# Kernel tuning notes

Hardware: AMD Instinct MI355X
Metric: run time of the kernel (lower is better)

## Reference

```python
import jax, jax.numpy as jnp
import numpy as np

B, H, W, C = 16, 64, 64, 256
C8 = C // 8

def setup_inputs() -> dict:
    key = jax.random.key(0)
    ks = jax.random.split(key, 8)
    return {
        "x": jax.random.normal(ks[0], (B, H, W, C), dtype=jnp.float32),
        "Wf": jax.random.normal(ks[1], (C, C8), dtype=jnp.float32) * 0.05,
        "Wg": jax.random.normal(ks[2], (C, C8), dtype=jnp.float32) * 0.05,
        "Wh": jax.random.normal(ks[3], (C, C), dtype=jnp.float32) * 0.05,
        "bf": jax.random.normal(ks[4], (C8,), dtype=jnp.float32) * 0.05,
        "bg": jax.random.normal(ks[5], (C8,), dtype=jnp.float32) * 0.05,
        "bh": jax.random.normal(ks[6], (C,), dtype=jnp.float32) * 0.05,
        "gamma": jax.random.normal(ks[7], (1,), dtype=jnp.float32) * 0.05,
    }

def reference(x, Wf, Wg, Wh, bf, bg, bh, gamma):
    # 1x1 convs == per-pixel channel matmuls (NHWC)
    f = jnp.einsum('bhwc,cd->bhwd', x, Wf) + bf  # [B,H,W,C/8]
    g = jnp.einsum('bhwc,cd->bhwd', x, Wg) + bg  # [B,H,W,C/8]
    h = jnp.einsum('bhwc,cd->bhwd', x, Wh) + bh  # [B,H,W,C]
    b = x.shape[0]
    # K.batch_flatten flattens all non-batch dims -> attention over BATCH dim
    gf = g.reshape(b, -1)                      # [B, HWC/8]
    ff = f.reshape(b, -1)                      # [B, HWC/8]
    hf = h.reshape(b, -1)                      # [B, HWC]
    s = gf @ ff.T                              # [B, B]
    beta = jax.nn.softmax(s, axis=-1)          # softmax over batch axis
    o = (beta @ hf).reshape(x.shape)           # [B,H,W,C]
    # activation=None -> linear; gamma-scaled residual
    return gamma * o + x
```

## Files before the change

kernel.cpp:

```cpp
#include <hip/hip_runtime.h>

typedef __attribute__((ext_vector_type(4))) float  f4;
typedef __attribute__((ext_vector_type(8))) short  short8;
typedef __attribute__((ext_vector_type(4))) float  f32x4;
typedef __attribute__((ext_vector_type(2))) unsigned int u32x2;

static __device__ __forceinline__ unsigned short f2bf(float f) {
    unsigned u = __builtin_bit_cast(unsigned, f);
    unsigned r = (u + 0x7FFFu + ((u >> 16) & 1u)) >> 16;
    return (unsigned short)r;
}
static __device__ __forceinline__ float bf2f(unsigned short h) {
    return __builtin_bit_cast(float, ((unsigned)h) << 16);
}

__global__ __launch_bounds__(256) void k_setup(const float* __restrict__ Wh,
                                               const float* __restrict__ bh,
                                               const float* __restrict__ Wf,
                                               const float* __restrict__ Wg,
                                               const float* __restrict__ gamma,
                                               unsigned short* __restrict__ WhT,
                                               float* __restrict__ gb,
                                               unsigned short* __restrict__ Wfg_hi,
                                               unsigned short* __restrict__ Wfg_lo) {
    __shared__ float T[8 * 260];
    const int t = threadIdx.x, b = blockIdx.x;
    const float g = gamma[0];
    if (b < 32) {
        const int c0 = b * 8;
        const int cr = t >> 5, q = t & 31;
        f4 v0 = *(const f4*)(Wh + (c0 + cr) * 256 + q * 8);
        f4 v1 = *(const f4*)(Wh + (c0 + cr) * 256 + q * 8 + 4);
        *(f4*)(T + cr * 260 + q * 8)     = v0;
        *(f4*)(T + cr * 260 + q * 8 + 4) = v1;
        __syncthreads();
        short8 o;
        #pragma unroll
        for (int j = 0; j < 8; ++j) o[j] = (short)f2bf(g * T[j * 260 + t]);
        *(short8*)(WhT + t * 256 + c0) = o;
    } else {
        gb[t] = g * bh[t];
        const int n = t >> 2, cq = t & 3;
        const float* Wsrc = (n < 32) ? Wf : Wg;
        const int nn = n & 31;
        #pragma unroll
        for (int c8 = 0; c8 < 8; ++c8) {
            short8 h8, l8;
            #pragma unroll
            for (int k = 0; k < 8; ++k) {
                const int c = cq * 64 + c8 * 8 + k;
                const float v = Wsrc[c * 32 + nn];
                const unsigned short h = f2bf(v);
                h8[k] = (short)h;
                l8[k] = (short)f2bf(v - bf2f(h));
            }
            *(short8*)(Wfg_hi + n * 256 + cq * 64 + c8 * 8) = h8;
            *(short8*)(Wfg_lo + n * 256 + cq * 64 + c8 * 8) = l8;
        }
    }
}

__global__ __launch_bounds__(256, 2) void ka(const float* __restrict__ x,
                                             const unsigned short* __restrict__ Wfg_hi,
                                             const unsigned short* __restrict__ Wfg_lo,
                                             const float* __restrict__ bfv,
                                             const float* __restrict__ bgv,
                                             float* __restrict__ s_part) {
    __shared__ __align__(16) unsigned char smem[65536];

    const int t = threadIdx.x, w = t >> 6, l = t & 63;
    const int p = blockIdx.x * 4 + w;

    f4 xr[16];
    #pragma unroll
    for (int j = 0; j < 16; ++j)
        xr[j] = *(const f4*)(x + (((j << 12) + p) << 8) + l * 4);
    #pragma unroll
    for (int j = 0; j < 16; ++j) {
        const int r = j * 4 + w;
        int bo = r * 512 + l * 8;
        bo ^= (r & 7) << 4;
        const unsigned short h0 = f2bf(xr[j][0]), h1 = f2bf(xr[j][1]);
        const unsigned short h2 = f2bf(xr[j][2]), h3 = f2bf(xr[j][3]);
        u32x2 ph, pl;
        ph[0] = ((unsigned)h1 << 16) | h0;
        ph[1] = ((unsigned)h3 << 16) | h2;
        const unsigned short e0 = f2bf(xr[j][0] - bf2f(h0));
        const unsigned short e1 = f2bf(xr[j][1] - bf2f(h1));
        const unsigned short e2 = f2bf(xr[j][2] - bf2f(h2));
        const unsigned short e3 = f2bf(xr[j][3] - bf2f(h3));
        pl[0] = ((unsigned)e1 << 16) | e0;
        pl[1] = ((unsigned)e3 << 16) | e2;
        *(u32x2*)(smem + bo)         = ph;
        *(u32x2*)(smem + 32768 + bo) = pl;
    }
    __syncthreads();

    const int lrow = l & 15;
    const int kfe  = (l >> 4) * 8;
    const int ncol = w * 16 + lrow;
    f32x4 acc[4];
    #pragma unroll
    for (int mt = 0; mt < 4; ++mt) acc[mt] = (f32x4){0.f, 0.f, 0.f, 0.f};

    #pragma unroll
    for (int k0 = 0; k0 < 256; k0 += 32) {
        const short8 bh_ = *(const short8*)(Wfg_hi + ncol * 256 + k0 + kfe);
        const short8 bl_ = *(const short8*)(Wfg_lo + ncol * 256 + k0 + kfe);
        short8 ah[4], al[4];
        #pragma unroll
        for (int mt = 0; mt < 4; ++mt) {
            const int row = mt * 16 + lrow;
            int bo = row * 512 + (k0 + kfe) * 2;
            bo ^= (row & 7) << 4;
            ah[mt] = *(const short8*)(smem + bo);
            al[mt] = *(const short8*)(smem + 32768 + bo);
        }
        #pragma unroll
        for (int mt = 0; mt < 4; ++mt) {
            acc[mt] = __builtin_amdgcn_mfma_f32_16x16x32_bf16(ah[mt], bh_, acc[mt], 0, 0, 0);
            acc[mt] = __builtin_amdgcn_mfma_f32_16x16x32_bf16(al[mt], bh_, acc[mt], 0, 0, 0);
            acc[mt] = __builtin_amdgcn_mfma_f32_16x16x32_bf16(ah[mt], bl_, acc[mt], 0, 0, 0);
        }
    }
    __syncthreads();

    float* FG = (float*)smem;
    const float bias = (ncol < 32) ? bfv[ncol] : bgv[ncol - 32];
    #pragma unroll
    for (int mt = 0; mt < 4; ++mt)
        #pragma unroll
        for (int jj = 0; jj < 4; ++jj) {
            const int row = mt * 16 + (l >> 4) * 4 + jj;
            FG[row * 68 + ncol] = acc[mt][jj] + bias;
        }
    __syncthreads();

    const int si = t >> 4, sj = t & 15;
    float sacc = 0.f;
    #pragma unroll
    for (int q = 0; q < 4; ++q) {
        const float* Gp = FG + (si * 4 + q) * 68 + 32;
        const float* Fp = FG + (sj * 4 + q) * 68;
        #pragma unroll
        for (int d4 = 0; d4 < 8; ++d4) {
            f4 gv = *(const f4*)(Gp + d4 * 4);
            f4 fv = *(const f4*)(Fp + d4 * 4);
            sacc += gv[0] * fv[0] + gv[1] * fv[1] + gv[2] * fv[2] + gv[3] * fv[3];
        }
    }
    s_part[blockIdx.x * 256 + si * 16 + sj] = sacc;
}

__global__ __launch_bounds__(256) void kb1(const float* __restrict__ s_part,
                                           float* __restrict__ s_red) {
    const int t = threadIdx.x, b = blockIdx.x;
    float a = 0.f;
    #pragma unroll
    for (int k = 0; k < 16; ++k) a += s_part[(b * 16 + k) * 256 + t];
    s_red[b * 256 + t] = a;
}

__global__ __launch_bounds__(1024) void kb2(const float* __restrict__ s_red,
                                            float* __restrict__ beta) {
    __shared__ float red[4 * 256];
    __shared__ float srow[256];
    __shared__ float erow[256];
    const int t = threadIdx.x;
    const int pair = t & 255;
    const int qr = t >> 8;
    float a = 0.f;
    #pragma unroll
    for (int b = qr * 16; b < qr * 16 + 16; ++b) a += s_red[b * 256 + pair];
    red[qr * 256 + pair] = a;
    __syncthreads();
    float s = 0.f, e = 0.f;
    if (t < 256) {
        s = red[pair] + red[256 + pair] + red[512 + pair] + red[768 + pair];
        srow[pair] = s;
    }
    __syncthreads();
    if (t < 256) {
        const int i = pair >> 4;
        float m = srow[i * 16];
        #pragma unroll
        for (int j = 1; j < 16; ++j) m = fmaxf(m, srow[i * 16 + j]);
        e = expf(s - m);
        erow[pair] = e;
    }
    __syncthreads();
    if (t < 256) {
        const int i = pair >> 4;
        float sum = 0.f;
        #pragma unroll
        for (int j = 0; j < 16; ++j) sum += erow[i * 16 + j];
        beta[pair] = e / sum;
    }
}

__global__ __launch_bounds__(256, 2) void kc(const float* __restrict__ x,
                                             const unsigned short* __restrict__ WhT,
                                             const float* __restrict__ gb,
                                             const float* __restrict__ beta,
                                             float* __restrict__ out) {
    __shared__ __align__(16) unsigned char smem[33024];

    const int t = threadIdx.x;
    const int w = t >> 6;
    const int l = t & 63;
    const int p0 = blockIdx.x * 4;
    const int p  = p0 + w;
    const int cbase = l * 4;

    f4 xr[16];
    #pragma unroll
    for (int j = 0; j < 16; ++j)
        xr[j] = *(const f4*)(x + (((j << 12) + p) << 8) + cbase);
    #pragma unroll
    for (int i = 0; i < 16; ++i) {
        f4 a = {0.f, 0.f, 0.f, 0.f};
        #pragma unroll
        for (int j = 0; j < 16; ++j) {
            const float bij = beta[i * 16 + j];
            a += xr[j] * bij;
        }
        const int r = i * 4 + w;
        int bo = r * 512 + l * 8;
        bo ^= (r & 7) << 4;
        u32x2 packed;
        packed[0] = ((unsigned)f2bf(a[1]) << 16) | f2bf(a[0]);
        packed[1] = ((unsigned)f2bf(a[3]) << 16) | f2bf(a[2]);
        *(u32x2*)(smem + bo) = packed;
    }
    __syncthreads();

    f32x4 acc[4][4];
    #pragma unroll
    for (int mt = 0; mt < 4; ++mt)
        #pragma unroll
        for (int nt = 0; nt < 4; ++nt) acc[mt][nt] = (f32x4){0.f, 0.f, 0.f, 0.f};

    const int n0 = w * 64;
    const int lrow = l & 15;
    const int hi = l >> 4;
    const int kf = hi * 8;
    #pragma unroll
    for (int k0 = 0; k0 < 256; k0 += 32) {
        short8 af[4], bfr[4];
        #pragma unroll
        for (int mt = 0; mt < 4; ++mt) {
            const int row = mt * 16 + lrow;
            int bo = row * 512 + (k0 + kf) * 2;
            bo ^= (row & 7) << 4;
            af[mt] = *(const short8*)(smem + bo);
        }
        #pragma unroll
        for (int nt = 0; nt < 4; ++nt) {
            const int d = n0 + nt * 16 + lrow;
            bfr[nt] = *(const short8*)(WhT + d * 256 + k0 + kf);
        }
        #pragma unroll
        for (int mt = 0; mt < 4; ++mt)
            #pragma unroll
            for (int nt = 0; nt < 4; ++nt)
                acc[mt][nt] = __builtin_amdgcn_mfma_f32_16x16x32_bf16(
                    af[mt], bfr[nt], acc[mt][nt], 0, 0, 0);
    }

    float* cst = (float*)smem;
    const f4 gb4 = *(const f4*)(gb + cbase);
    #pragma unroll
    for (int h = 0; h < 2; ++h) {
        __syncthreads();
        #pragma unroll
        for (int mt2 = 0; mt2 < 2; ++mt2) {
            const int mt = h * 2 + mt2;
            #pragma unroll
            for (int nt = 0; nt < 4; ++nt)
                #pragma unroll
                for (int j = 0; j < 4; ++j) {
                    const int rl = mt2 * 16 + hi * 4 + j;
                    cst[rl * 258 + n0 + nt * 16 + lrow] = acc[mt][nt][j];
                }
        }
        __syncthreads();
        #pragma unroll
        for (int rr = 0; rr < 8; ++rr) {
            const int rl = rr * 4 + w;
            const int i  = h * 8 + rr;
            f4 o = *(const f4*)(cst + rl * 258 + cbase);
            o += gb4 + xr[i];
            *(f4*)(out + (((i << 12) + p) << 8) + cbase) = o;
        }
    }
}

extern "C" void kernel_launch(void* const* d_in, const int* in_sizes, int n_in,
                              void* d_out, int out_size, void* d_ws, size_t ws_size,
                              hipStream_t stream) {
    const float* x     = (const float*)d_in[0];
    const float* Wf    = (const float*)d_in[1];
    const float* Wg    = (const float*)d_in[2];
    const float* Wh    = (const float*)d_in[3];
    const float* bfv   = (const float*)d_in[4];
    const float* bgv   = (const float*)d_in[5];
    const float* bhv   = (const float*)d_in[6];
    const float* gamma = (const float*)d_in[7];
    float* out = (float*)d_out;

    char* ws = (char*)d_ws;
    unsigned short* WhT = (unsigned short*)ws;
    float* gb     = (float*)(ws + 131072);
    float* beta   = (float*)(ws + 132096);
    float* s_part = (float*)(ws + 133120);
    unsigned short* Wfg_hi = (unsigned short*)(ws + 1181696);
    unsigned short* Wfg_lo = (unsigned short*)(ws + 1214464);
    float* s_red  = (float*)(ws + 1181696);

    k_setup<<<dim3(33), dim3(256), 0, stream>>>(Wh, bhv, Wf, Wg, gamma, WhT, gb, Wfg_hi, Wfg_lo);
    ka<<<dim3(1024), dim3(256), 0, stream>>>(x, Wfg_hi, Wfg_lo, bfv, bgv, s_part);
    kb1<<<dim3(64), dim3(256), 0, stream>>>(s_part, s_red);
    kb2<<<dim3(1), dim3(1024), 0, stream>>>(s_red, beta);
    kc<<<dim3(1024), dim3(256), 0, stream>>>(x, WhT, gb, beta, out);
}
```

Baseline: 86.61 us.

## Halve kc tile to two pixels per block to raise occupancy

The final kernel now processes 2 pixels per block instead of 4, doubling the grid, halving shared memory, and raising launch bounds to 5 blocks per SM. x is no longer held in registers across the GEMM; the residual is re-read from global memory in the epilogue, and output uses nontemporal stores. This trades a second read of x and twice the WhT fetches per pixel for lower register and LDS pressure and more waves in flight.

```diff
diff --git a/kernel.cpp b/kernel.cpp
--- a/kernel.cpp
+++ b/kernel.cpp
@@ -1,6 +1,7 @@
 #include <hip/hip_runtime.h>
 
 typedef __attribute__((ext_vector_type(4))) float  f4;
+typedef __attribute__((ext_vector_type(2))) float  f2;
 typedef __attribute__((ext_vector_type(8))) short  short8;
 typedef __attribute__((ext_vector_type(4))) float  f32x4;
 typedef __attribute__((ext_vector_type(2))) unsigned int u32x2;
@@ -198,57 +199,57 @@
     }
 }
 
-__global__ __launch_bounds__(256, 2) void kc(const float* __restrict__ x,
+__global__ __launch_bounds__(256, 5) void kc(const float* __restrict__ x,
                                              const unsigned short* __restrict__ WhT,
                                              const float* __restrict__ gb,
                                              const float* __restrict__ beta,
                                              float* __restrict__ out) {
-    __shared__ __align__(16) unsigned char smem[33024];
+    __shared__ __align__(16) unsigned char smem[16896];
 
     const int t = threadIdx.x;
     const int w = t >> 6;
     const int l = t & 63;
-    const int p0 = blockIdx.x * 4;
-    const int p  = p0 + w;
-    const int cbase = l * 4;
-
-    f4 xr[16];
-    #pragma unroll
-    for (int j = 0; j < 16; ++j)
-        xr[j] = *(const f4*)(x + (((j << 12) + p) << 8) + cbase);
-    #pragma unroll
-    for (int i = 0; i < 16; ++i) {
-        f4 a = {0.f, 0.f, 0.f, 0.f};
-        #pragma unroll
-        for (int j = 0; j < 16; ++j) {
-            const float bij = beta[i * 16 + j];
-            a += xr[j] * bij;
-        }
-        const int r = i * 4 + w;
-        int bo = r * 512 + l * 8;
-        bo ^= (r & 7) << 4;
-        u32x2 packed;
-        packed[0] = ((unsigned)f2bf(a[1]) << 16) | f2bf(a[0]);
-        packed[1] = ((unsigned)f2bf(a[3]) << 16) | f2bf(a[2]);
-        *(u32x2*)(smem + bo) = packed;
-    }
-    __syncthreads();
-
-    f32x4 acc[4][4];
-    #pragma unroll
-    for (int mt = 0; mt < 4; ++mt)
+    const int p0 = blockIdx.x * 2;
+
+    {
+        const int px  = w >> 1;
+        const int cb2 = ((w & 1) * 64 + l) * 2;
+        const int p   = p0 + px;
+        f2 xr[16];
+        #pragma unroll
+        for (int j = 0; j < 16; ++j)
+            xr[j] = *(const f2*)(x + (((j << 12) + p) << 8) + cb2);
+        #pragma unroll
+        for (int i = 0; i < 16; ++i) {
+            f2 a = {0.f, 0.f};
+            #pragma unroll
+            for (int j = 0; j < 16; ++j) {
+                const float bij = beta[i * 16 + j];
+                a += xr[j] * bij;
+            }
+            const int r = i * 2 + px;
+            int bo = r * 512 + cb2 * 2;
+            bo ^= (r & 7) << 4;
+            *(unsigned*)(smem + bo) = ((unsigned)f2bf(a[1]) << 16) | f2bf(a[0]);
+        }
+    }
+    __syncthreads();
+
+    f32x4 acc[2][4];
+    #pragma unroll
+    for (int mt = 0; mt < 2; ++mt)
         #pragma unroll
         for (int nt = 0; nt < 4; ++nt) acc[mt][nt] = (f32x4){0.f, 0.f, 0.f, 0.f};
 
     const int n0 = w * 64;
     const int lrow = l & 15;
-    const int hi = l >> 4;
-    const int kf = hi * 8;
+    const int hi4 = l >> 4;
+    const int kf = hi4 * 8;
     #pragma unroll
     for (int k0 = 0; k0 < 256; k0 += 32) {
-        short8 af[4], bfr[4];
-        #pragma unroll
-        for (int mt = 0; mt < 4; ++mt) {
+        short8 af[2], bfr[4];
+        #pragma unroll
+        for (int mt = 0; mt < 2; ++mt) {
             const int row = mt * 16 + lrow;
             int bo = row * 512 + (k0 + kf) * 2;
             bo ^= (row & 7) << 4;
@@ -260,7 +261,7 @@
             bfr[nt] = *(const short8*)(WhT + d * 256 + k0 + kf);
         }
         #pragma unroll
-        for (int mt = 0; mt < 4; ++mt)
+        for (int mt = 0; mt < 2; ++mt)
             #pragma unroll
             for (int nt = 0; nt < 4; ++nt)
                 acc[mt][nt] = __builtin_amdgcn_mfma_f32_16x16x32_bf16(
@@ -268,29 +269,25 @@
     }
 
     float* cst = (float*)smem;
-    const f4 gb4 = *(const f4*)(gb + cbase);
+    const f4 gb4 = *(const f4*)(gb + l * 4);
     #pragma unroll
     for (int h = 0; h < 2; ++h) {
         __syncthreads();
         #pragma unroll
-        for (int mt2 = 0; mt2 < 2; ++mt2) {
-            const int mt = h * 2 + mt2;
+        for (int nt = 0; nt < 4; ++nt)
             #pragma unroll
-            for (int nt = 0; nt < 4; ++nt)
-                #pragma unroll
-                for (int j = 0; j < 4; ++j) {
-                    const int rl = mt2 * 16 + hi * 4 + j;
-                    cst[rl * 258 + n0 + nt * 16 + lrow] = acc[mt][nt][j];
-                }
-        }
+            for (int j = 0; j < 4; ++j)
+                cst[(hi4 * 4 + j) * 258 + n0 + nt * 16 + lrow] = acc[h][nt][j];
         __syncthreads();
         #pragma unroll
-        for (int rr = 0; rr < 8; ++rr) {
-            const int rl = rr * 4 + w;
-            const int i  = h * 8 + rr;
-            f4 o = *(const f4*)(cst + rl * 258 + cbase);
-            o += gb4 + xr[i];
-            *(f4*)(out + (((i << 12) + p) << 8) + cbase) = o;
+        for (int rr = 0; rr < 4; ++rr) {
+            const int rl = w * 4 + rr;
+            const int rg = h * 16 + rl;
+            const int i  = rg >> 1, pxe = rg & 1;
+            const int idx = (((i << 12) + p0 + pxe) << 8) + l * 4;
+            f4 o = *(const f4*)(cst + rl * 258 + l * 4);
+            o += gb4 + *(const f4*)(x + idx);
+            __builtin_nontemporal_store(o, (f4*)(out + idx));
         }
     }
 }
@@ -321,5 +318,5 @@
     ka<<<dim3(1024), dim3(256), 0, stream>>>(x, Wfg_hi, Wfg_lo, bfv, bgv, s_part);
     kb1<<<dim3(64), dim3(256), 0, stream>>>(s_part, s_red);
     kb2<<<dim3(1), dim3(1024), 0, stream>>>(s_red, beta);
-    kc<<<dim3(1024), dim3(256), 0, stream>>>(x, WhT, gb, beta, out);
-}
+    kc<<<dim3(2048), dim3(256), 0, stream>>>(x, WhT, gb, beta, out);
+}
```

Result: slower. 97.50 us (+12.6%).

## Raise kc occupancy: stage beta in LDS, prefetch WhT, reload x in epilogue

Applied to the files above, without the earlier changes.

Raises the kernel's launch-bounds occupancy hint from 2 to 3 blocks per SM. To make that fit, the 16 x registers are no longer kept live into the epilogue; the residual x values are re-read from global memory there instead. The beta matrix is copied into shared memory once, and each coefficient row is read as four float4 vectors rather than as scalar global loads. WhT fragments for the next k-step are register-prefetched ahead of the MFMA loop, and output writes become nontemporal stores. The trade-off is extra global reads of x in exchange for better latency hiding and a tighter register budget.

```diff
diff --git a/kernel.cpp b/kernel.cpp
--- a/kernel.cpp
+++ b/kernel.cpp
@@ -1,6 +1,7 @@
 #include <hip/hip_runtime.h>
 
 typedef __attribute__((ext_vector_type(4))) float  f4;
+typedef __attribute__((ext_vector_type(2))) float  f2;
 typedef __attribute__((ext_vector_type(8))) short  short8;
 typedef __attribute__((ext_vector_type(4))) float  f32x4;
 typedef __attribute__((ext_vector_type(2))) unsigned int u32x2;
@@ -198,12 +199,13 @@
     }
 }
 
-__global__ __launch_bounds__(256, 2) void kc(const float* __restrict__ x,
+__global__ __launch_bounds__(256, 3) void kc(const float* __restrict__ x,
                                              const unsigned short* __restrict__ WhT,
                                              const float* __restrict__ gb,
                                              const float* __restrict__ beta,
                                              float* __restrict__ out) {
-    __shared__ __align__(16) unsigned char smem[33024];
+    __shared__ __align__(16) unsigned char smem[34048];
+    float* beta_l = (float*)(smem + 33024);
 
     const int t = threadIdx.x;
     const int w = t >> 6;
@@ -216,13 +218,22 @@
     #pragma unroll
     for (int j = 0; j < 16; ++j)
         xr[j] = *(const f4*)(x + (((j << 12) + p) << 8) + cbase);
+    if (t < 64) *(f4*)(beta_l + t * 4) = *(const f4*)(beta + t * 4);
+    __syncthreads();
+
     #pragma unroll
     for (int i = 0; i < 16; ++i) {
+        f4 bv0 = *(const f4*)(beta_l + i * 16);
+        f4 bv1 = *(const f4*)(beta_l + i * 16 + 4);
+        f4 bv2 = *(const f4*)(beta_l + i * 16 + 8);
+        f4 bv3 = *(const f4*)(beta_l + i * 16 + 12);
         f4 a = {0.f, 0.f, 0.f, 0.f};
         #pragma unroll
-        for (int j = 0; j < 16; ++j) {
-            const float bij = beta[i * 16 + j];
-            a += xr[j] * bij;
+        for (int j = 0; j < 4; ++j) {
+            a += xr[j]      * bv0[j];
+            a += xr[4 + j]  * bv1[j];
+            a += xr[8 + j]  * bv2[j];
+            a += xr[12 + j] * bv3[j];
         }
         const int r = i * 4 + w;
         int bo = r * 512 + l * 8;
@@ -244,9 +255,22 @@
     const int lrow = l & 15;
     const int hi = l >> 4;
     const int kf = hi * 8;
-    #pragma unroll
-    for (int k0 = 0; k0 < 256; k0 += 32) {
-        short8 af[4], bfr[4];
+    const unsigned short* wbase = WhT + (n0 + lrow) * 256 + kf;
+
+    short8 bcur[4], bnxt[4];
+    #pragma unroll
+    for (int nt = 0; nt < 4; ++nt)
+        bcur[nt] = *(const short8*)(wbase + nt * 16 * 256);
+
+    #pragma unroll
+    for (int ks = 0; ks < 8; ++ks) {
+        const int k0 = ks * 32;
+        if (ks < 7) {
+            #pragma unroll
+            for (int nt = 0; nt < 4; ++nt)
+                bnxt[nt] = *(const short8*)(wbase + nt * 16 * 256 + k0 + 32);
+        }
+        short8 af[4];
         #pragma unroll
         for (int mt = 0; mt < 4; ++mt) {
             const int row = mt * 16 + lrow;
@@ -255,16 +279,13 @@
             af[mt] = *(const short8*)(smem + bo);
         }
         #pragma unroll
-        for (int nt = 0; nt < 4; ++nt) {
-            const int d = n0 + nt * 16 + lrow;
-            bfr[nt] = *(const short8*)(WhT + d * 256 + k0 + kf);
-        }
-        #pragma unroll
         for (int mt = 0; mt < 4; ++mt)
             #pragma unroll
             for (int nt = 0; nt < 4; ++nt)
                 acc[mt][nt] = __builtin_amdgcn_mfma_f32_16x16x32_bf16(
-                    af[mt], bfr[nt], acc[mt][nt], 0, 0, 0);
+                    af[mt], bcur[nt], acc[mt][nt], 0, 0, 0);
+        #pragma unroll
+        for (int nt = 0; nt < 4; ++nt) bcur[nt] = bnxt[nt];
     }
 
     float* cst = (float*)smem;
@@ -287,10 +308,12 @@
         #pragma unroll
         for (int rr = 0; rr < 8; ++rr) {
             const int rl = rr * 4 + w;
-            const int i  = h * 8 + rr;
+            const int rg = h * 32 + rl;
+            const int i  = rg >> 2, q = rg & 3;
+            const int idx = (((i << 12) + p0 + q) << 8) + cbase;
             f4 o = *(const f4*)(cst + rl * 258 + cbase);
-            o += gb4 + xr[i];
-            *(f4*)(out + (((i << 12) + p) << 8) + cbase) = o;
+            o += gb4 + *(const f4*)(x + idx);
+            __builtin_nontemporal_store(o, (f4*)(out + idx));
         }
     }
 }
```

Result: faster. 79.81 us (-7.9%).
